# Kernel tuning notes

Hardware: AMD Instinct MI355X
Metric: run time of the kernel (lower is better)

The kernel has to match this reference:

```python
import jax, jax.numpy as jnp
import numpy as np

B, N, G = 8, 512, 16          # images, proposals/img, gt boxes/img
C = 91                        # num classes (incl background)
FEAT = 256 * 7 * 7            # pooled RoI feature dim = 12544
REP = 1024                    # TwoMLPHead representation size
FG, BG = 0.5, 0.5             # fg/bg IoU thresholds
BBOX_W = (10.0, 10.0, 5.0, 5.0)
BETA = 1.0 / 9.0              # smooth-L1 beta


def setup_inputs() -> dict:
    key = jax.random.key(0)
    ks = jax.random.split(key, 12)
    # valid xyxy boxes inside an ~800x800 image
    tl = jax.random.uniform(ks[0], (B, N, 2), minval=0.0, maxval=700.0)
    wh = jax.random.uniform(ks[1], (B, N, 2), minval=8.0, maxval=128.0)
    proposals = jnp.concatenate([tl, tl + wh], axis=-1)
    gtl = jax.random.uniform(ks[2], (B, G, 2), minval=0.0, maxval=700.0)
    gwh = jax.random.uniform(ks[3], (B, G, 2), minval=8.0, maxval=128.0)
    gt_boxes = jnp.concatenate([gtl, gtl + gwh], axis=-1)
    gt_labels = jax.random.randint(ks[4], (B, G), 1, C)  # foreground labels 1..C-1
    P = N + G
    features = jax.random.normal(ks[5], (B * P, FEAT), dtype=jnp.float32)
    s = 0.01
    return {
        'proposals': proposals, 'gt_boxes': gt_boxes, 'features': features,
        'W1': jax.random.normal(ks[6], (FEAT, REP), jnp.float32) * s,
        'b1': jnp.zeros((REP,), jnp.float32),
        'W2': jax.random.normal(ks[7], (REP, REP), jnp.float32) * s,
        'b2': jnp.zeros((REP,), jnp.float32),
        'Wcls': jax.random.normal(ks[8], (REP, C), jnp.float32) * s,
        'bcls': jnp.zeros((C,), jnp.float32),
        'Wbox': jax.random.normal(ks[9], (REP, C * 4), jnp.float32) * s,
        'bbox': jnp.zeros((C * 4,), jnp.float32),
        'gt_labels': gt_labels,
    }


def _box_iou(gt, pr):
    # gt: [B,G,4], pr: [B,P,4] -> [B,G,P]
    area_g = (gt[..., 2] - gt[..., 0]) * (gt[..., 3] - gt[..., 1])
    area_p = (pr[..., 2] - pr[..., 0]) * (pr[..., 3] - pr[..., 1])
    lt = jnp.maximum(gt[:, :, None, :2], pr[:, None, :, :2])
    rb = jnp.minimum(gt[:, :, None, 2:], pr[:, None, :, 2:])
    wh = jnp.clip(rb - lt, 0.0)
    inter = wh[..., 0] * wh[..., 1]
    return inter / (area_g[:, :, None] + area_p[:, None, :] - inter)


def _encode(ref, gt):
    # torchvision BoxCoder.encode_single; ref/gt: [...,4]
    wx, wy, ww, wh = BBOX_W
    ew = ref[..., 2] - ref[..., 0]; eh = ref[..., 3] - ref[..., 1]
    ex = ref[..., 0] + 0.5 * ew;    ey = ref[..., 1] + 0.5 * eh
    gw = gt[..., 2] - gt[..., 0];   gh = gt[..., 3] - gt[..., 1]
    gx = gt[..., 0] + 0.5 * gw;     gy = gt[..., 1] + 0.5 * gh
    return jnp.stack([
        wx * (gx - ex) / ew, wy * (gy - ey) / eh,
        ww * jnp.log(gw / ew), wh * jnp.log(gh / eh)], axis=-1)


def reference(proposals, gt_boxes, features, W1, b1, W2, b2, Wcls, bcls, Wbox, bbox, gt_labels):
    # add_gt_proposals
    props = jnp.concatenate([proposals, gt_boxes], axis=1)  # [B,P,4]
    # assign_targets_to_proposals (Matcher, allow_low_quality_matches=False)
    iou = _box_iou(gt_boxes, props)                          # [B,G,P]
    matched_vals = iou.max(axis=1)                           # [B,P]
    matched_idx = iou.argmax(axis=1)                         # [B,P]
    labels = jnp.take_along_axis(gt_labels, matched_idx, axis=1)
    labels = jnp.where(matched_vals < BG, 0, labels)                         # background
    labels = jnp.where((matched_vals >= BG) & (matched_vals < FG), -1, labels)  # ignore
    matched_gt = jnp.take_along_axis(gt_boxes, matched_idx[..., None], axis=1)  # [B,P,4]
    reg_targets = _encode(props, matched_gt).reshape(-1, 4)  # [R,4]
    labels = labels.reshape(-1)                               # [R]

    # TwoMLPHead + FastRCNNPredictor
    x = jax.nn.relu(features @ W1 + b1)
    x = jax.nn.relu(x @ W2 + b2)
    class_logits = x @ Wcls + bcls                            # [R,C]
    box_regression = (x @ Wbox + bbox).reshape(-1, C, 4)      # [R,C,4]

    # fastrcnn_loss (all proposals; ignored labels (-1) masked from CE)
    R = class_logits.shape[0]
    valid = (labels >= 0).astype(class_logits.dtype)
    safe_lab = jnp.clip(labels, 0, C - 1)
    logp = jax.nn.log_softmax(class_logits, axis=-1)
    nll = -jnp.take_along_axis(logp, safe_lab[:, None], axis=1)[:, 0]
    classification_loss = (nll * valid).sum() / jnp.maximum(valid.sum(), 1.0)

    pos = (labels > 0).astype(class_logits.dtype)
    pred = jnp.take_along_axis(box_regression, safe_lab[:, None, None], axis=1)[:, 0]  # [R,4]
    d = jnp.abs(pred - reg_targets)
    sl1 = jnp.where(d < BETA, 0.5 * d * d / BETA, d - 0.5 * BETA).sum(-1)
    box_loss = (sl1 * pos).sum() / R

    return jnp.stack([classification_loss, box_loss])
```

## Files before the change

kernel.cpp:

```cpp
#include <hip/hip_runtime.h>
#include <cstdint>
#include <cstddef>

#define BQ   8
#define NP   512
#define GQ   16
#define PP   528
#define RT   4224
#define CC   91
#define FEATD 12544
#define REPD 1024
#define NH   512
#define NHU  455
#define BETA (1.0f/9.0f)
#define WSC  64.0f

typedef float f32x4 __attribute__((ext_vector_type(4)));
typedef int   v8i  __attribute__((ext_vector_type(8)));
typedef float v16f __attribute__((ext_vector_type(16)));

__device__ __forceinline__ unsigned short f2bf(float f) {
  unsigned int x = __float_as_uint(f);
  unsigned int r = (x + 0x7fffu + ((x >> 16) & 1u)) >> 16;
  return (unsigned short)r;
}
__device__ __forceinline__ float bf2f(unsigned short u) {
  return __uint_as_float((unsigned int)u << 16);
}
__device__ __forceinline__ unsigned char f2fp8(float f) {
  return (unsigned char)(__builtin_amdgcn_cvt_pk_fp8_f32(f, 0.0f, 0, false) & 0xff);
}

__device__ __forceinline__ void ld_lds16(const void* g, void* l) {
  __builtin_amdgcn_global_load_lds(
      (const __attribute__((address_space(1))) void*)g,
      (__attribute__((address_space(3))) void*)l, 16, 0, 0);
}

constexpr size_t O_W1T = 0;
constexpr size_t SZ_W1T = (size_t)FEATD * REPD;
constexpr size_t O_W2T = O_W1T + SZ_W1T;
constexpr size_t SZ_W2T = (size_t)REPD * REPD;
constexpr size_t O_WH  = O_W2T + SZ_W2T;
constexpr size_t SZ_WH = (size_t)NH * REPD;
constexpr size_t O_BH  = O_WH + SZ_WH;
constexpr size_t SZ_BH = (size_t)NH * 4;
constexpr size_t O_X1  = O_BH + SZ_BH;
constexpr size_t SZ_X1 = (size_t)RT * REPD;
constexpr size_t O_X2  = O_X1 + SZ_X1;
constexpr size_t O_LAB = O_X2 + SZ_X1;
constexpr size_t O_TGT = O_LAB + (size_t)RT * 4;
constexpr size_t O_NLL = O_TGT + (size_t)RT * 16;
constexpr size_t O_VC  = O_NLL + (size_t)RT * 4;
constexpr size_t O_SL1 = O_VC + (size_t)RT * 4;
constexpr size_t O_PART = ((O_SL1 + (size_t)RT * 4) + 255) & ~(size_t)255;
constexpr size_t SZ_PART = (size_t)4 * RT * REPD * 2;
constexpr size_t O_F8 = O_PART + SZ_PART;

__device__ __forceinline__ void t32(const float* __restrict__ in, unsigned char* __restrict__ out,
                                    int K, int N, int row_off, int out_ld,
                                    int bx, int by, int t, float (*tile)[33]) {
  int tx = t & 31, ty = t >> 5;
  int n0 = bx * 32, k0 = by * 32;
#pragma unroll
  for (int i = 0; i < 4; ++i) {
    int k = k0 + ty + i * 8, n = n0 + tx;
    if (k < K && n < N) tile[ty + i * 8][tx] = in[(size_t)k * N + n];
  }
  __syncthreads();
#pragma unroll
  for (int i = 0; i < 4; ++i) {
    int n = n0 + ty + i * 8, k = k0 + tx;
    if (n < N && k < K) out[(size_t)(n + row_off) * out_ld + k] = f2fp8(tile[tx][ty + i * 8] * WSC);
  }
}

#define NB_CV ((RT * FEATD / 4) / 256)
#define NB_W1 ((REPD/32)*(FEATD/32))
#define NB_W2 ((REPD/32)*(REPD/32))
#define NB_WC (3*(REPD/32))
#define NB_WB (12*(REPD/32))
#define NB_HI 230
#define NB_MT 17
#define NB_PREP (NB_CV+NB_W1+NB_W2+NB_WC+NB_WB+NB_HI+NB_MT)

__global__ void prep(const float* __restrict__ feat, unsigned int* __restrict__ feat8,
                     const float* __restrict__ W1, const float* __restrict__ W2,
                     const float* __restrict__ Wcls, const float* __restrict__ Wbox,
                     const float* __restrict__ bcls, const float* __restrict__ bbox,
                     const float* __restrict__ proposals, const float* __restrict__ gt_boxes,
                     const int* __restrict__ gt_labels,
                     unsigned char* __restrict__ W1t, unsigned char* __restrict__ W2t,
                     unsigned char* __restrict__ Wh, float* __restrict__ bh,
                     int* __restrict__ labels, float* __restrict__ tgts) {
  __shared__ float tile[32][33];
  int b = blockIdx.x, t = threadIdx.x;
  if (b < NB_CV) {
    long i = (long)b * 256 + t;
    float4 f = ((const float4*)feat)[i];
    unsigned int r = (unsigned int)__builtin_amdgcn_cvt_pk_fp8_f32(f.x, f.y, 0, false);
    r = (unsigned int)__builtin_amdgcn_cvt_pk_fp8_f32(f.z, f.w, (int)r, true);
    feat8[i] = r;
    return;
  }
  b -= NB_CV;
  if (b < NB_W1) { t32(W1, W1t, FEATD, REPD, 0, FEATD, b % (REPD/32), b / (REPD/32), t, tile); return; }
  b -= NB_W1;
  if (b < NB_W2) { t32(W2, W2t, REPD, REPD, 0, REPD, b % 32, b / 32, t, tile); return; }
  b -= NB_W2;
  if (b < NB_WC) { t32(Wcls, Wh, REPD, CC, 0, REPD, b % 3, b / 3, t, tile); return; }
  b -= NB_WC;
  if (b < NB_WB) { t32(Wbox, Wh, REPD, 4 * CC, CC, REPD, b % 12, b / 12, t, tile); return; }
  b -= NB_WB;
  if (b < NB_HI) {
    int idx = b * 256 + t;
    const int npad = (NH - NHU) * REPD;
    if (idx < npad) Wh[(size_t)NHU * REPD + idx] = 0;
    else {
      int i2 = idx - npad;
      if (i2 < NH) bh[i2] = (i2 < CC) ? bcls[i2] : (i2 < NHU ? bbox[i2 - CC] : 0.0f);
    }
    return;
  }
  b -= NB_HI;
  int r = b * 256 + t;
  if (r >= RT) return;
  int bi_ = r / PP, p = r % PP;
  float x0, y0, x1, y1;
  if (p < NP) {
    const float* qq = proposals + ((size_t)bi_ * NP + p) * 4;
    x0 = qq[0]; y0 = qq[1]; x1 = qq[2]; y1 = qq[3];
  } else {
    const float* qq = gt_boxes + ((size_t)bi_ * GQ + (p - NP)) * 4;
    x0 = qq[0]; y0 = qq[1]; x1 = qq[2]; y1 = qq[3];
  }
  float ap = (x1 - x0) * (y1 - y0);
  float best = -1.0f; int bg = 0;
#pragma unroll
  for (int g = 0; g < GQ; ++g) {
    const float* gb = gt_boxes + ((size_t)bi_ * GQ + g) * 4;
    float gx0 = gb[0], gy0 = gb[1], gx1 = gb[2], gy1 = gb[3];
    float ag = (gx1 - gx0) * (gy1 - gy0);
    float iw = fmaxf(fminf(gx1, x1) - fmaxf(gx0, x0), 0.0f);
    float ih = fmaxf(fminf(gy1, y1) - fmaxf(gy0, y0), 0.0f);
    float inter = iw * ih;
    float iou = inter / (ag + ap - inter);
    if (iou > best) { best = iou; bg = g; }
  }
  int lab = gt_labels[bi_ * GQ + bg];
  if (best < 0.5f) lab = 0;
  labels[r] = lab;
  const float* gb = gt_boxes + ((size_t)bi_ * GQ + bg) * 4;
  float ew = x1 - x0, eh = y1 - y0;
  float ex = x0 + 0.5f * ew, ey = y0 + 0.5f * eh;
  float gw = gb[2] - gb[0], gh = gb[3] - gb[1];
  float gx = gb[0] + 0.5f * gw, gy = gb[1] + 0.5f * gh;
  tgts[r * 4 + 0] = 10.0f * (gx - ex) / ew;
  tgts[r * 4 + 1] = 10.0f * (gy - ey) / eh;
  tgts[r * 4 + 2] = 5.0f * logf(gw / ew);
  tgts[r * 4 + 3] = 5.0f * logf(gh / eh);
}

__global__ __launch_bounds__(256, 4)
void gemm_f8(const unsigned char* __restrict__ A, const unsigned char* __restrict__ Bt,
             unsigned short* __restrict__ P, int M, int Nc, int K, int Kspl,
             int n_nblk, int n_my, int npairs) {
  __shared__ unsigned char As[2 * 8192];
  __shared__ unsigned char Bs[2 * 8192];

  const int g = blockIdx.x;
  const int xcd = g & 7;
  const int kix = g >> 3;
  const int n  = kix % n_nblk;
  const int pi = kix / n_nblk;
  const int p  = pi * 8 + xcd;
  if (p >= npairs) return;
  const int y  = p % n_my;
  const int kz = p / n_my;
  const int m0 = y * 128, n0 = n * 128;

  const int tid = threadIdx.x;
  const int w = tid >> 6, L = tid & 63;
  const int l31 = L & 31, h = L >> 5;
  const int wr = (w >> 1) * 64, wc = (w & 1) * 64;
  const size_t kbase = (size_t)kz * Kspl;

  const int srow = L & 15, schk = (L >> 4) * 16;
  const int sg = 2 * w;
  const int sgo0 = sg * 1024, sgo1 = (sg + 1) * 1024;
  const unsigned char* gA0 = A  + (size_t)(m0 + sg * 16 + srow) * K + kbase + schk;
  const unsigned char* gA1 = A  + (size_t)(m0 + (sg + 1) * 16 + srow) * K + kbase + schk;
  const unsigned char* gB0 = Bt + (size_t)(n0 + sg * 16 + srow) * K + kbase + schk;
  const unsigned char* gB1 = Bt + (size_t)(n0 + (sg + 1) * 16 + srow) * K + kbase + schk;

  int ab[2], bb[2];
#pragma unroll
  for (int i = 0; i < 2; ++i) {
    int ra = wr + i * 32 + l31;
    ab[i] = (ra >> 4) * 1024 + (ra & 15) * 16 + h * 512;
    int rb = wc + i * 32 + l31;
    bb[i] = (rb >> 4) * 1024 + (rb & 15) * 16 + h * 512;
  }

  ld_lds16(gA0, &As[sgo0]);
  ld_lds16(gA1, &As[sgo1]);
  ld_lds16(gB0, &Bs[sgo0]);
  ld_lds16(gB1, &Bs[sgo1]);

  v16f acc[2][2] = {};
  const int nk = Kspl >> 6;
  int cur = 0;
  for (int kb = 0; kb < nk; ++kb) {
    const int cb = cur << 13;
    const int nb = cb ^ 8192;
    if (kb + 1 < nk) {
      const int ko = (kb + 1) * 64;
      ld_lds16(gA0 + ko, &As[nb + sgo0]);
      ld_lds16(gA1 + ko, &As[nb + sgo1]);
      ld_lds16(gB0 + ko, &Bs[nb + sgo0]);
      ld_lds16(gB1 + ko, &Bs[nb + sgo1]);
      asm volatile("s_waitcnt vmcnt(4)" ::: "memory");
    } else {
      asm volatile("s_waitcnt vmcnt(0)" ::: "memory");
    }
    __builtin_amdgcn_sched_barrier(0);
    __builtin_amdgcn_s_barrier();

    v8i a[2], b[2];
#pragma unroll
    for (int i = 0; i < 2; ++i) {
      int4 alo = *(const int4*)&As[cb + ab[i]];
      int4 ahi = *(const int4*)&As[cb + ab[i] + 256];
      a[i] = (v8i){alo.x, alo.y, alo.z, alo.w, ahi.x, ahi.y, ahi.z, ahi.w};
      int4 blo = *(const int4*)&Bs[cb + bb[i]];
      int4 bhi = *(const int4*)&Bs[cb + bb[i] + 256];
      b[i] = (v8i){blo.x, blo.y, blo.z, blo.w, bhi.x, bhi.y, bhi.z, bhi.w};
    }
#pragma unroll
    for (int i = 0; i < 2; ++i)
#pragma unroll
      for (int j = 0; j < 2; ++j)
        acc[i][j] = __builtin_amdgcn_mfma_scale_f32_32x32x64_f8f6f4(
            a[i], b[j], acc[i][j], 0, 0, 0, 127, 0, 127);

    asm volatile("s_waitcnt lgkmcnt(0)" ::: "memory");
    __builtin_amdgcn_sched_barrier(0);
    __builtin_amdgcn_s_barrier();
    cur ^= 1;
  }

  unsigned short* Pz = P + (size_t)kz * M * Nc;
#pragma unroll
  for (int i = 0; i < 2; ++i) {
#pragma unroll
    for (int j = 0; j < 2; ++j) {
      int colb = n0 + wc + j * 32 + l31;
#pragma unroll
      for (int r = 0; r < 16; ++r) {
        int row = m0 + wr + i * 32 + (r & 3) + 8 * (r >> 2) + 4 * h;
        Pz[(size_t)row * Nc + colb] = f2bf(acc[i][j][r]);
      }
    }
  }
}

template <int S>
__global__ void reduce_fp8k(const unsigned short* __restrict__ P, const float* __restrict__ bias,
                            unsigned int* __restrict__ outp, long MN4, int nc4) {
  long i = (long)blockIdx.x * blockDim.x + threadIdx.x;
  long stride = (long)gridDim.x * blockDim.x;
  const ushort4* P4 = (const ushort4*)P;
  const float4* B4 = (const float4*)bias;
  for (; i < MN4; i += stride) {
    float vx = 0, vy = 0, vz = 0, vw = 0;
#pragma unroll
    for (int s = 0; s < S; ++s) {
      ushort4 u = P4[s * MN4 + i];
      vx += bf2f(u.x); vy += bf2f(u.y); vz += bf2f(u.z); vw += bf2f(u.w);
    }
    float4 b = B4[i % nc4];
    vx = fmaxf(vx * (1.0f / WSC) + b.x, 0.0f);
    vy = fmaxf(vy * (1.0f / WSC) + b.y, 0.0f);
    vz = fmaxf(vz * (1.0f / WSC) + b.z, 0.0f);
    vw = fmaxf(vw * (1.0f / WSC) + b.w, 0.0f);
    unsigned int r = (unsigned int)__builtin_amdgcn_cvt_pk_fp8_f32(vx, vy, 0, false);
    r = (unsigned int)__builtin_amdgcn_cvt_pk_fp8_f32(vz, vw, (int)r, true);
    outp[i] = r;
  }
}

__global__ void loss_row(const unsigned short* __restrict__ P, const float* __restrict__ bh,
                         const int* __restrict__ labels, const float* __restrict__ tgts,
                         float* __restrict__ nll_v, float* __restrict__ vc_v,
                         float* __restrict__ sl1_v) {
  int r = blockIdx.x;
  int l = threadIdx.x;
  const size_t SL = (size_t)RT * NH;
  const unsigned short* p0 = P + (size_t)r * NH;
#define COLV(c) ((bf2f(p0[(c)]) + bf2f(p0[SL + (c)]) + bf2f(p0[2 * SL + (c)]) + \
                  bf2f(p0[3 * SL + (c)])) * (1.0f / WSC) + bh[(c)])
  float v1 = COLV(l);
  float v2 = (l < CC - 64) ? COLV(64 + l) : -3.4e38f;
  float m = fmaxf(v1, v2);
#pragma unroll
  for (int o = 32; o; o >>= 1) m = fmaxf(m, __shfl_xor(m, o));
  float e = __expf(v1 - m) + ((l < CC - 64) ? __expf(v2 - m) : 0.0f);
#pragma unroll
  for (int o = 32; o; o >>= 1) e += __shfl_xor(e, o);
  if (l == 0) {
    float lse = m + __logf(e);
    int lab = labels[r];
    int sl = lab < 0 ? 0 : (lab > CC - 1 ? CC - 1 : lab);
    float valid = (lab >= 0) ? 1.0f : 0.0f;
    nll_v[r] = (lse - COLV(sl)) * valid;
    vc_v[r] = valid;
    float s = 0.0f;
#pragma unroll
    for (int d = 0; d < 4; ++d) {
      float pd = COLV(CC + sl * 4 + d);
      float ad = fabsf(pd - tgts[r * 4 + d]);
      s += (ad < BETA) ? 0.5f * ad * ad / BETA : ad - 0.5f * BETA;
    }
    sl1_v[r] = (lab > 0) ? s : 0.0f;
  }
#undef COLV
}

__global__ void reduce_final(const float* __restrict__ nll_v, const float* __restrict__ vc_v,
                             const float* __restrict__ sl1_v, float* __restrict__ out) {
  __shared__ float s1[256], s2[256], s3[256];
  int t = threadIdx.x;
  float a = 0, b = 0, c = 0;
  for (int i = t; i < RT; i += 256) { a += nll_v[i]; b += vc_v[i]; c += sl1_v[i]; }
  s1[t] = a; s2[t] = b; s3[t] = c;
  __syncthreads();
  for (int o = 128; o; o >>= 1) {
    if (t < o) { s1[t] += s1[t + o]; s2[t] += s2[t + o]; s3[t] += s3[t + o]; }
    __syncthreads();
  }
  if (t == 0) {
    out[0] = s1[0] / fmaxf(s2[0], 1.0f);
    out[1] = s3[0] / (float)RT;
  }
}

extern "C" void kernel_launch(void* const* d_in, const int* in_sizes, int n_in,
                              void* d_out, int out_size, void* d_ws, size_t ws_size,
                              hipStream_t stream) {
  const float* proposals = (const float*)d_in[0];
  const float* gt_boxes  = (const float*)d_in[1];
  const float* features  = (const float*)d_in[2];
  const float* W1   = (const float*)d_in[3];
  const float* b1   = (const float*)d_in[4];
  const float* W2   = (const float*)d_in[5];
  const float* b2   = (const float*)d_in[6];
  const float* Wcls = (const float*)d_in[7];
  const float* bcls = (const float*)d_in[8];
  const float* Wbox = (const float*)d_in[9];
  const float* bbox = (const float*)d_in[10];
  const int* gt_labels = (const int*)d_in[11];
  float* out = (float*)d_out;

  char* ws = (char*)d_ws;
  unsigned char* W1t = (unsigned char*)(ws + O_W1T);
  unsigned char* W2t = (unsigned char*)(ws + O_W2T);
  unsigned char* Wh  = (unsigned char*)(ws + O_WH);
  float* bh          = (float*)(ws + O_BH);
  unsigned char* x1  = (unsigned char*)(ws + O_X1);
  unsigned char* x2  = (unsigned char*)(ws + O_X2);
  int* labels        = (int*)(ws + O_LAB);
  float* tgts        = (float*)(ws + O_TGT);
  float* nll_v       = (float*)(ws + O_NLL);
  float* vc_v        = (float*)(ws + O_VC);
  float* sl1_v       = (float*)(ws + O_SL1);
  unsigned short* part = (unsigned short*)(ws + O_PART);
  unsigned char* feat8 = (unsigned char*)(ws + O_F8);

  prep<<<NB_PREP, 256, 0, stream>>>(features, (unsigned int*)feat8, W1, W2, Wcls, Wbox,
                                    bcls, bbox, proposals, gt_boxes, gt_labels,
                                    W1t, W2t, Wh, bh, labels, tgts);

  gemm_f8<<<1088, 256, 0, stream>>>(feat8, W1t, part, RT, REPD, FEATD, FEATD / 4,
                                    8, 33, 132);
  reduce_fp8k<4><<<2048, 256, 0, stream>>>(part, b1, (unsigned int*)x1,
                                           (long)RT * REPD / 4, REPD / 4);

  gemm_f8<<<576, 256, 0, stream>>>(x1, W2t, part, RT, REPD, REPD, REPD / 2,
                                   8, 33, 66);
  reduce_fp8k<2><<<2048, 256, 0, stream>>>(part, b2, (unsigned int*)x2,
                                           (long)RT * REPD / 4, REPD / 4);

  gemm_f8<<<544, 256, 0, stream>>>(x2, Wh, part, RT, NH, REPD, REPD / 4,
                                   4, 33, 132);

  loss_row<<<RT, 64, 0, stream>>>(part, bh, labels, tgts, nll_v, vc_v, sl1_v);
  reduce_final<<<1, 256, 0, stream>>>(nll_v, vc_v, sl1_v, out);
}
```

Before: 521.9 us.

## Double K-tile depth in FP8 GEMM, halve split-K, stagger K start per block

The FP8 MFMA GEMM now stages 128-wide K tiles (32KB LDS per operand, double-buffered) instead of 64-wide tiles, and runs two MFMA sub-steps per barrier pair. Launch bounds drop to 2 blocks per CU. The first GEMM's split-K goes from 4 to 2, which halves the partial-sum traffic written and reread by the reduction. A per-N-block staggered starting K offset (wrapping modulo the tile count) is meant to spread concurrent blocks across different K regions and reduce cache and channel contention. The cost is lower occupancy and fewer blocks in the largest GEMM.

```diff
diff --git a/kernel.cpp b/kernel.cpp
--- a/kernel.cpp
+++ b/kernel.cpp
@@ -161,12 +161,12 @@
   tgts[r * 4 + 3] = 5.0f * logf(gh / eh);
 }
 
-__global__ __launch_bounds__(256, 4)
+__global__ __launch_bounds__(256, 2)
 void gemm_f8(const unsigned char* __restrict__ A, const unsigned char* __restrict__ Bt,
              unsigned short* __restrict__ P, int M, int Nc, int K, int Kspl,
-             int n_nblk, int n_my, int npairs) {
-  __shared__ unsigned char As[2 * 8192];
-  __shared__ unsigned char Bs[2 * 8192];
+             int n_nblk, int n_my, int npairs, int stag) {
+  __shared__ unsigned char As[2 * 16384];
+  __shared__ unsigned char Bs[2 * 16384];
 
   const int g = blockIdx.x;
   const int xcd = g & 7;
@@ -185,69 +185,83 @@
   const int wr = (w >> 1) * 64, wc = (w & 1) * 64;
   const size_t kbase = (size_t)kz * Kspl;
 
-  const int srow = L & 15, schk = (L >> 4) * 16;
-  const int sg = 2 * w;
-  const int sgo0 = sg * 1024, sgo1 = (sg + 1) * 1024;
-  const unsigned char* gA0 = A  + (size_t)(m0 + sg * 16 + srow) * K + kbase + schk;
-  const unsigned char* gA1 = A  + (size_t)(m0 + (sg + 1) * 16 + srow) * K + kbase + schk;
-  const unsigned char* gB0 = Bt + (size_t)(n0 + sg * 16 + srow) * K + kbase + schk;
-  const unsigned char* gB1 = Bt + (size_t)(n0 + (sg + 1) * 16 + srow) * K + kbase + schk;
-
-  int ab[2], bb[2];
+  const int srow = L & 7, schk = (L >> 3) * 16;
+  const long K8 = (long)8 * K;
+  const unsigned char* gAr = A  + (size_t)(m0 + w * 32 + srow) * K + kbase + schk;
+  const unsigned char* gBr = Bt + (size_t)(n0 + w * 32 + srow) * K + kbase + schk;
+  const unsigned char* gA0 = gAr;            const unsigned char* gB0 = gBr;
+  const unsigned char* gA1 = gAr + K8;       const unsigned char* gB1 = gBr + K8;
+  const unsigned char* gA2 = gAr + 2 * K8;   const unsigned char* gB2 = gBr + 2 * K8;
+  const unsigned char* gA3 = gAr + 3 * K8;   const unsigned char* gB3 = gBr + 3 * K8;
+  const int lo0 = w * 4096;
+
+#define STAGE(kb2, bufo) do {                                   \
+    const int _ko = (kb2) * 128;                                \
+    ld_lds16(gA0 + _ko, &As[(bufo) + lo0]);                     \
+    ld_lds16(gA1 + _ko, &As[(bufo) + lo0 + 1024]);              \
+    ld_lds16(gA2 + _ko, &As[(bufo) + lo0 + 2048]);              \
+    ld_lds16(gA3 + _ko, &As[(bufo) + lo0 + 3072]);              \
+    ld_lds16(gB0 + _ko, &Bs[(bufo) + lo0]);                     \
+    ld_lds16(gB1 + _ko, &Bs[(bufo) + lo0 + 1024]);              \
+    ld_lds16(gB2 + _ko, &Bs[(bufo) + lo0 + 2048]);              \
+    ld_lds16(gB3 + _ko, &Bs[(bufo) + lo0 + 3072]);              \
+  } while (0)
+
+  int aoff[2], boff[2];
 #pragma unroll
   for (int i = 0; i < 2; ++i) {
     int ra = wr + i * 32 + l31;
-    ab[i] = (ra >> 4) * 1024 + (ra & 15) * 16 + h * 512;
+    aoff[i] = (ra >> 3) * 1024 + (ra & 7) * 16 + h * 256;
     int rb = wc + i * 32 + l31;
-    bb[i] = (rb >> 4) * 1024 + (rb & 15) * 16 + h * 512;
-  }
-
-  ld_lds16(gA0, &As[sgo0]);
-  ld_lds16(gA1, &As[sgo1]);
-  ld_lds16(gB0, &Bs[sgo0]);
-  ld_lds16(gB1, &Bs[sgo1]);
+    boff[i] = (rb >> 3) * 1024 + (rb & 7) * 16 + h * 256;
+  }
+
+  const int nk2 = Kspl >> 7;
+  int kb2 = n * stag;
+  STAGE(kb2, 0);
 
   v16f acc[2][2] = {};
-  const int nk = Kspl >> 6;
   int cur = 0;
-  for (int kb = 0; kb < nk; ++kb) {
-    const int cb = cur << 13;
-    const int nb = cb ^ 8192;
-    if (kb + 1 < nk) {
-      const int ko = (kb + 1) * 64;
-      ld_lds16(gA0 + ko, &As[nb + sgo0]);
-      ld_lds16(gA1 + ko, &As[nb + sgo1]);
-      ld_lds16(gB0 + ko, &Bs[nb + sgo0]);
-      ld_lds16(gB1 + ko, &Bs[nb + sgo1]);
-      asm volatile("s_waitcnt vmcnt(4)" ::: "memory");
+  for (int t = 0; t < nk2; ++t) {
+    const int cb = cur << 14;
+    const int nb = cb ^ 16384;
+    int kn = kb2 + 1; if (kn == nk2) kn = 0;
+    if (t + 1 < nk2) {
+      STAGE(kn, nb);
+      asm volatile("s_waitcnt vmcnt(8)" ::: "memory");
     } else {
       asm volatile("s_waitcnt vmcnt(0)" ::: "memory");
     }
     __builtin_amdgcn_sched_barrier(0);
     __builtin_amdgcn_s_barrier();
 
-    v8i a[2], b[2];
-#pragma unroll
-    for (int i = 0; i < 2; ++i) {
-      int4 alo = *(const int4*)&As[cb + ab[i]];
-      int4 ahi = *(const int4*)&As[cb + ab[i] + 256];
-      a[i] = (v8i){alo.x, alo.y, alo.z, alo.w, ahi.x, ahi.y, ahi.z, ahi.w};
-      int4 blo = *(const int4*)&Bs[cb + bb[i]];
-      int4 bhi = *(const int4*)&Bs[cb + bb[i] + 256];
-      b[i] = (v8i){blo.x, blo.y, blo.z, blo.w, bhi.x, bhi.y, bhi.z, bhi.w};
-    }
-#pragma unroll
-    for (int i = 0; i < 2; ++i)
-#pragma unroll
-      for (int j = 0; j < 2; ++j)
-        acc[i][j] = __builtin_amdgcn_mfma_scale_f32_32x32x64_f8f6f4(
-            a[i], b[j], acc[i][j], 0, 0, 0, 127, 0, 127);
+#pragma unroll
+    for (int s = 0; s < 2; ++s) {
+      v8i a[2], b[2];
+#pragma unroll
+      for (int i = 0; i < 2; ++i) {
+        int4 alo = *(const int4*)&As[cb + aoff[i] + s * 512];
+        int4 ahi = *(const int4*)&As[cb + aoff[i] + s * 512 + 128];
+        a[i] = (v8i){alo.x, alo.y, alo.z, alo.w, ahi.x, ahi.y, ahi.z, ahi.w};
+        int4 blo = *(const int4*)&Bs[cb + boff[i] + s * 512];
+        int4 bhi = *(const int4*)&Bs[cb + boff[i] + s * 512 + 128];
+        b[i] = (v8i){blo.x, blo.y, blo.z, blo.w, bhi.x, bhi.y, bhi.z, bhi.w};
+      }
+#pragma unroll
+      for (int i = 0; i < 2; ++i)
+#pragma unroll
+        for (int j = 0; j < 2; ++j)
+          acc[i][j] = __builtin_amdgcn_mfma_scale_f32_32x32x64_f8f6f4(
+              a[i], b[j], acc[i][j], 0, 0, 0, 127, 0, 127);
+    }
 
     asm volatile("s_waitcnt lgkmcnt(0)" ::: "memory");
     __builtin_amdgcn_sched_barrier(0);
     __builtin_amdgcn_s_barrier();
     cur ^= 1;
-  }
+    kb2 = kn;
+  }
+#undef STAGE
 
   unsigned short* Pz = P + (size_t)kz * M * Nc;
 #pragma unroll
@@ -380,18 +394,18 @@
                                     bcls, bbox, proposals, gt_boxes, gt_labels,
                                     W1t, W2t, Wh, bh, labels, tgts);
 
-  gemm_f8<<<1088, 256, 0, stream>>>(feat8, W1t, part, RT, REPD, FEATD, FEATD / 4,
-                                    8, 33, 132);
-  reduce_fp8k<4><<<2048, 256, 0, stream>>>(part, b1, (unsigned int*)x1,
+  gemm_f8<<<576, 256, 0, stream>>>(feat8, W1t, part, RT, REPD, FEATD, FEATD / 2,
+                                   8, 33, 66, 6);
+  reduce_fp8k<2><<<2048, 256, 0, stream>>>(part, b1, (unsigned int*)x1,
                                            (long)RT * REPD / 4, REPD / 4);
 
   gemm_f8<<<576, 256, 0, stream>>>(x1, W2t, part, RT, REPD, REPD, REPD / 2,
-                                   8, 33, 66);
+                                   8, 33, 66, 0);
   reduce_fp8k<2><<<2048, 256, 0, stream>>>(part, b2, (unsigned int*)x2,
                                            (long)RT * REPD / 4, REPD / 4);
 
   gemm_f8<<<544, 256, 0, stream>>>(x2, Wh, part, RT, NH, REPD, REPD / 4,
-                                   4, 33, 132);
+                                   4, 33, 132, 0);
 
   loss_row<<<RT, 64, 0, stream>>>(part, bh, labels, tgts, nll_v, vc_v, sl1_v);
   reduce_final<<<1, 256, 0, stream>>>(nll_v, vc_v, sl1_v, out);
```

Result: slower. 566.1 us (+8.5%).

## Pre-tile FP8 operands into contiguous 8KB LDS-image blocks for GEMM loads

Applied to the files above, without the earlier changes.

All FP8 GEMM operands (features, W1, W2, head weights, and intermediate activations) are now written in a blocked layout. Each 128-row by 64-k tile is stored as one contiguous 8KB image that matches the LDS layout. The GEMM staging then issues fully contiguous 16-byte global-to-LDS loads instead of strided row loads. This is meant to improve global memory coalescing and cut address arithmetic in the main loop. In exchange, the prep kernel and reduce kernels take on more complex scatter indexing and an LDS staging pass for the feature conversion.

```diff
diff --git a/kernel.cpp b/kernel.cpp
--- a/kernel.cpp
+++ b/kernel.cpp
@@ -35,6 +35,12 @@
   __builtin_amdgcn_global_load_lds(
       (const __attribute__((address_space(1))) void*)g,
       (__attribute__((address_space(3))) void*)l, 16, 0, 0);
+}
+
+__device__ __forceinline__ size_t img_off(int row, int kb, int KT) {
+  return (size_t)((row >> 7) * KT + (kb >> 6)) * 8192
+       + (size_t)((((row >> 5) & 3) << 11) + (((kb >> 4) & 3) << 9)
+                  + ((row & 31) << 4) + (kb & 15));
 }
 
 constexpr size_t O_W1T = 0;
@@ -58,7 +64,7 @@
 constexpr size_t O_F8 = O_PART + SZ_PART;
 
 __device__ __forceinline__ void t32(const float* __restrict__ in, unsigned char* __restrict__ out,
-                                    int K, int N, int row_off, int out_ld,
+                                    int K, int N, int row_off, int KT,
                                     int bx, int by, int t, float (*tile)[33]) {
   int tx = t & 31, ty = t >> 5;
   int n0 = bx * 32, k0 = by * 32;
@@ -71,11 +77,12 @@
 #pragma unroll
   for (int i = 0; i < 4; ++i) {
     int n = n0 + ty + i * 8, k = k0 + tx;
-    if (n < N && k < K) out[(size_t)(n + row_off) * out_ld + k] = f2fp8(tile[tx][ty + i * 8] * WSC);
-  }
-}
-
-#define NB_CV ((RT * FEATD / 4) / 256)
+    if (n < N && k < K)
+      out[img_off(n + row_off, k, KT)] = f2fp8(tile[tx][ty + i * 8] * WSC);
+  }
+}
+
+#define NB_CV ((RT/128)*(FEATD/64))
 #define NB_W1 ((REPD/32)*(FEATD/32))
 #define NB_W2 ((REPD/32)*(REPD/32))
 #define NB_WC (3*(REPD/32))
@@ -84,7 +91,7 @@
 #define NB_MT 17
 #define NB_PREP (NB_CV+NB_W1+NB_W2+NB_WC+NB_WB+NB_HI+NB_MT)
 
-__global__ void prep(const float* __restrict__ feat, unsigned int* __restrict__ feat8,
+__global__ void prep(const float* __restrict__ feat, unsigned char* __restrict__ feat8,
                      const float* __restrict__ W1, const float* __restrict__ W2,
                      const float* __restrict__ Wcls, const float* __restrict__ Wbox,
                      const float* __restrict__ bcls, const float* __restrict__ bbox,
@@ -94,29 +101,44 @@
                      unsigned char* __restrict__ Wh, float* __restrict__ bh,
                      int* __restrict__ labels, float* __restrict__ tgts) {
   __shared__ float tile[32][33];
+  __shared__ unsigned char cvbuf[8192];
   int b = blockIdx.x, t = threadIdx.x;
   if (b < NB_CV) {
-    long i = (long)b * 256 + t;
-    float4 f = ((const float4*)feat)[i];
-    unsigned int r = (unsigned int)__builtin_amdgcn_cvt_pk_fp8_f32(f.x, f.y, 0, false);
-    r = (unsigned int)__builtin_amdgcn_cvt_pk_fp8_f32(f.z, f.w, (int)r, true);
-    feat8[i] = r;
+    int yb = b / (FEATD / 64), kt = b % (FEATD / 64);
+    const float* src = feat + (size_t)(yb * 128) * FEATD + kt * 64;
+#pragma unroll
+    for (int p = 0; p < 8; ++p) {
+      int lr = p * 16 + (t >> 4);
+      int kb = (t & 15) * 4;
+      float4 f = *(const float4*)(src + (size_t)lr * FEATD + kb);
+      unsigned int r = (unsigned int)__builtin_amdgcn_cvt_pk_fp8_f32(f.x, f.y, 0, false);
+      r = (unsigned int)__builtin_amdgcn_cvt_pk_fp8_f32(f.z, f.w, (int)r, true);
+      int o = (((lr >> 5) & 3) << 11) + (((kb >> 4) & 3) << 9) + ((lr & 31) << 4) + (kb & 15);
+      *(unsigned int*)&cvbuf[o] = r;
+    }
+    __syncthreads();
+    int4* dst = (int4*)(feat8 + (size_t)b * 8192);
+    const int4* sb = (const int4*)cvbuf;
+    dst[t] = sb[t];
+    dst[256 + t] = sb[256 + t];
     return;
   }
   b -= NB_CV;
-  if (b < NB_W1) { t32(W1, W1t, FEATD, REPD, 0, FEATD, b % (REPD/32), b / (REPD/32), t, tile); return; }
+  if (b < NB_W1) { t32(W1, W1t, FEATD, REPD, 0, FEATD/64, b % (REPD/32), b / (REPD/32), t, tile); return; }
   b -= NB_W1;
-  if (b < NB_W2) { t32(W2, W2t, REPD, REPD, 0, REPD, b % 32, b / 32, t, tile); return; }
+  if (b < NB_W2) { t32(W2, W2t, REPD, REPD, 0, REPD/64, b % 32, b / 32, t, tile); return; }
   b -= NB_W2;
-  if (b < NB_WC) { t32(Wcls, Wh, REPD, CC, 0, REPD, b % 3, b / 3, t, tile); return; }
+  if (b < NB_WC) { t32(Wcls, Wh, REPD, CC, 0, REPD/64, b % 3, b / 3, t, tile); return; }
   b -= NB_WC;
-  if (b < NB_WB) { t32(Wbox, Wh, REPD, 4 * CC, CC, REPD, b % 12, b / 12, t, tile); return; }
+  if (b < NB_WB) { t32(Wbox, Wh, REPD, 4 * CC, CC, REPD/64, b % 12, b / 12, t, tile); return; }
   b -= NB_WB;
   if (b < NB_HI) {
     int idx = b * 256 + t;
     const int npad = (NH - NHU) * REPD;
-    if (idx < npad) Wh[(size_t)NHU * REPD + idx] = 0;
-    else {
+    if (idx < npad) {
+      int row = NHU + (idx >> 10), k = idx & 1023;
+      Wh[img_off(row, k, REPD/64)] = 0;
+    } else {
       int i2 = idx - npad;
       if (i2 < NH) bh[i2] = (i2 < CC) ? bcls[i2] : (i2 < NHU ? bbox[i2 - CC] : 0.0f);
     }
@@ -162,8 +184,8 @@
 }
 
 __global__ __launch_bounds__(256, 4)
-void gemm_f8(const unsigned char* __restrict__ A, const unsigned char* __restrict__ Bt,
-             unsigned short* __restrict__ P, int M, int Nc, int K, int Kspl,
+void gemm_f8(const unsigned char* __restrict__ Aimg, const unsigned char* __restrict__ Bimg,
+             unsigned short* __restrict__ P, int M, int Nc, int KT, int nkt,
              int n_nblk, int n_my, int npairs) {
   __shared__ unsigned char As[2 * 8192];
   __shared__ unsigned char Bs[2 * 8192];
@@ -183,42 +205,35 @@
   const int w = tid >> 6, L = tid & 63;
   const int l31 = L & 31, h = L >> 5;
   const int wr = (w >> 1) * 64, wc = (w & 1) * 64;
-  const size_t kbase = (size_t)kz * Kspl;
-
-  const int srow = L & 15, schk = (L >> 4) * 16;
-  const int sg = 2 * w;
-  const int sgo0 = sg * 1024, sgo1 = (sg + 1) * 1024;
-  const unsigned char* gA0 = A  + (size_t)(m0 + sg * 16 + srow) * K + kbase + schk;
-  const unsigned char* gA1 = A  + (size_t)(m0 + (sg + 1) * 16 + srow) * K + kbase + schk;
-  const unsigned char* gB0 = Bt + (size_t)(n0 + sg * 16 + srow) * K + kbase + schk;
-  const unsigned char* gB1 = Bt + (size_t)(n0 + (sg + 1) * 16 + srow) * K + kbase + schk;
-
-  int ab[2], bb[2];
+
+  const int kt0 = kz * nkt;
+  const unsigned char* gA = Aimg + ((size_t)y * KT + kt0) * 8192 + w * 2048 + L * 16;
+  const unsigned char* gB = Bimg + ((size_t)n * KT + kt0) * 8192 + w * 2048 + L * 16;
+  const int lw = w * 2048;
+
+#define STAGE(it, bufo) do {                                    \
+    const size_t _go = (size_t)(it) * 8192;                     \
+    ld_lds16(gA + _go,        &As[(bufo) + lw]);                \
+    ld_lds16(gA + _go + 1024, &As[(bufo) + lw + 1024]);         \
+    ld_lds16(gB + _go,        &Bs[(bufo) + lw]);                \
+    ld_lds16(gB + _go + 1024, &Bs[(bufo) + lw + 1024]);         \
+  } while (0)
+
+  int aoff[2], boff[2];
 #pragma unroll
   for (int i = 0; i < 2; ++i) {
-    int ra = wr + i * 32 + l31;
-    ab[i] = (ra >> 4) * 1024 + (ra & 15) * 16 + h * 512;
-    int rb = wc + i * 32 + l31;
-    bb[i] = (rb >> 4) * 1024 + (rb & 15) * 16 + h * 512;
-  }
-
-  ld_lds16(gA0, &As[sgo0]);
-  ld_lds16(gA1, &As[sgo1]);
-  ld_lds16(gB0, &Bs[sgo0]);
-  ld_lds16(gB1, &Bs[sgo1]);
+    aoff[i] = (((w >> 1) * 2 + i) << 11) + (h << 10) + (l31 << 4);
+    boff[i] = (((w & 1) * 2 + i) << 11) + (h << 10) + (l31 << 4);
+  }
+
+  STAGE(0, 0);
 
   v16f acc[2][2] = {};
-  const int nk = Kspl >> 6;
   int cur = 0;
-  for (int kb = 0; kb < nk; ++kb) {
+  for (int it = 0; it < nkt; ++it) {
     const int cb = cur << 13;
-    const int nb = cb ^ 8192;
-    if (kb + 1 < nk) {
-      const int ko = (kb + 1) * 64;
-      ld_lds16(gA0 + ko, &As[nb + sgo0]);
-      ld_lds16(gA1 + ko, &As[nb + sgo1]);
-      ld_lds16(gB0 + ko, &Bs[nb + sgo0]);
-      ld_lds16(gB1 + ko, &Bs[nb + sgo1]);
+    if (it + 1 < nkt) {
+      STAGE(it + 1, cb ^ 8192);
       asm volatile("s_waitcnt vmcnt(4)" ::: "memory");
     } else {
       asm volatile("s_waitcnt vmcnt(0)" ::: "memory");
@@ -229,11 +244,11 @@
     v8i a[2], b[2];
 #pragma unroll
     for (int i = 0; i < 2; ++i) {
-      int4 alo = *(const int4*)&As[cb + ab[i]];
-      int4 ahi = *(const int4*)&As[cb + ab[i] + 256];
+      int4 alo = *(const int4*)&As[cb + aoff[i]];
+      int4 ahi = *(const int4*)&As[cb + aoff[i] + 512];
       a[i] = (v8i){alo.x, alo.y, alo.z, alo.w, ahi.x, ahi.y, ahi.z, ahi.w};
-      int4 blo = *(const int4*)&Bs[cb + bb[i]];
-      int4 bhi = *(const int4*)&Bs[cb + bb[i] + 256];
+      int4 blo = *(const int4*)&Bs[cb + boff[i]];
+      int4 bhi = *(const int4*)&Bs[cb + boff[i] + 512];
       b[i] = (v8i){blo.x, blo.y, blo.z, blo.w, bhi.x, bhi.y, bhi.z, bhi.w};
     }
 #pragma unroll
@@ -248,6 +263,7 @@
     __builtin_amdgcn_s_barrier();
     cur ^= 1;
   }
+#undef STAGE
 
   unsigned short* Pz = P + (size_t)kz * M * Nc;
 #pragma unroll
@@ -278,14 +294,16 @@
       ushort4 u = P4[s * MN4 + i];
       vx += bf2f(u.x); vy += bf2f(u.y); vz += bf2f(u.z); vw += bf2f(u.w);
     }
-    float4 b = B4[i % nc4];
+    float4 b = B4[i & (nc4 - 1)];
     vx = fmaxf(vx * (1.0f / WSC) + b.x, 0.0f);
     vy = fmaxf(vy * (1.0f / WSC) + b.y, 0.0f);
     vz = fmaxf(vz * (1.0f / WSC) + b.z, 0.0f);
     vw = fmaxf(vw * (1.0f / WSC) + b.w, 0.0f);
     unsigned int r = (unsigned int)__builtin_amdgcn_cvt_pk_fp8_f32(vx, vy, 0, false);
     r = (unsigned int)__builtin_amdgcn_cvt_pk_fp8_f32(vz, vw, (int)r, true);
-    outp[i] = r;
+    int rr = (int)(i >> 8);
+    int kb = ((int)i & 255) * 4;
+    outp[img_off(rr, kb, REPD / 64) >> 2] = r;
   }
 }
 
@@ -376,21 +394,21 @@
   unsigned short* part = (unsigned short*)(ws + O_PART);
   unsigned char* feat8 = (unsigned char*)(ws + O_F8);
 
-  prep<<<NB_PREP, 256, 0, stream>>>(features, (unsigned int*)feat8, W1, W2, Wcls, Wbox,
+  prep<<<NB_PREP, 256, 0, stream>>>(features, feat8, W1, W2, Wcls, Wbox,
                                     bcls, bbox, proposals, gt_boxes, gt_labels,
                                     W1t, W2t, Wh, bh, labels, tgts);
 
-  gemm_f8<<<1088, 256, 0, stream>>>(feat8, W1t, part, RT, REPD, FEATD, FEATD / 4,
+  gemm_f8<<<1088, 256, 0, stream>>>(feat8, W1t, part, RT, REPD, FEATD/64, 49,
                                     8, 33, 132);
   reduce_fp8k<4><<<2048, 256, 0, stream>>>(part, b1, (unsigned int*)x1,
                                            (long)RT * REPD / 4, REPD / 4);
 
-  gemm_f8<<<576, 256, 0, stream>>>(x1, W2t, part, RT, REPD, REPD, REPD / 2,
+  gemm_f8<<<576, 256, 0, stream>>>(x1, W2t, part, RT, REPD, REPD/64, 8,
                                    8, 33, 66);
   reduce_fp8k<2><<<2048, 256, 0, stream>>>(part, b2, (unsigned int*)x2,
                                            (long)RT * REPD / 4, REPD / 4);
 
-  gemm_f8<<<544, 256, 0, stream>>>(x2, Wh, part, RT, NH, REPD, REPD / 4,
+  gemm_f8<<<544, 256, 0, stream>>>(x2, Wh, part, RT, NH, REPD/64, 4,
                                    4, 33, 132);
 
   loss_row<<<RT, 64, 0, stream>>>(part, bh, labels, tgts, nll_v, vc_v, sl1_v);
```

Result: faster. 485.9 us (-6.9%).
